# Kernel tuning notes

Measured on AMD Instinct MI355X. Metric: run time of the kernel, lower is better.

## Reference

```python
import jax, jax.numpy as jnp
import numpy as np

N_DATA, N_NODES, N_EDGES = 64, 1000, 16000


def _lrelu(x):
    return jax.nn.leaky_relu(x, 0.01)


def _mlp2(x, W1, b1, W2, b2):
    # x: [B, Cin, N] -> two 1x1-conv (per-position linear) layers with LeakyReLU
    h = _lrelu(jnp.einsum('bcn,oc->bon', x, W1) + b1[None, :, None])
    return _lrelu(jnp.einsum('bcn,oc->bon', h, W2) + b2[None, :, None])


def setup_inputs():
    key = jax.random.key(0)
    ks = jax.random.split(key, 32)
    w = lambda k, s: jax.random.normal(k, s, jnp.float32) * 0.05
    return {
        'vertices': jax.random.normal(ks[0], (N_DATA, N_NODES, 11), jnp.float32),
        'edges': jax.random.randint(ks[1], (2, N_EDGES), 0, N_NODES),
        'x_W': w(ks[2], (8, 2)), 'x_b': w(ks[3], (8,)),
        'y_W': w(ks[4], (8, 2)), 'y_b': w(ks[5], (8,)),
        'th_W': w(ks[6], (8, 2)), 'th_b': w(ks[7], (8,)),
        'cfg_W1': w(ks[8], (32, 24)), 'cfg_b1': w(ks[9], (32,)),
        'cfg_W2': w(ks[10], (32, 32)), 'cfg_b2': w(ks[11], (32,)),
        'vtx_W1': w(ks[12], (32, 64)), 'vtx_b1': w(ks[13], (32,)),
        'vtx_W2': w(ks[14], (32, 32)), 'vtx_b2': w(ks[15], (32,)),
        'edg_W1': w(ks[16], (32, 68)), 'edg_b1': w(ks[17], (32,)),
        'edg_W2': w(ks[18], (32, 32)), 'edg_b2': w(ks[19], (32,)),
        'aft_W1': w(ks[20], (32, 32)), 'aft_b1': w(ks[21], (32,)),
        'aft_W2': w(ks[22], (32, 32)), 'aft_b2': w(ks[23], (32,)),
        'vo_W1': w(ks[24], (32, 32)), 'vo_b1': w(ks[25], (32,)),
        'vo_W2': w(ks[26], (1, 32)), 'vo_b2': w(ks[27], (1,)),
        'go_W': w(ks[28], (1, N_NODES)), 'go_b': w(ks[29], (1,)),
    }


def reference(vertices, edges, x_W, x_b, y_W, y_b, th_W, th_b,
              cfg_W1, cfg_b1, cfg_W2, cfg_b2, vtx_W1, vtx_b1, vtx_W2, vtx_b2,
              edg_W1, edg_b1, edg_W2, edg_b2, aft_W1, aft_b1, aft_W2, aft_b2,
              vo_W1, vo_b1, vo_W2, vo_b2, go_W, go_b):
    n_nodes = vertices.shape[1]
    src, dst = edges[0], edges[1]

    qk, q0, qg = vertices[..., 0:3], vertices[..., 3:6], vertices[..., 6:9]
    col = jnp.transpose(vertices[..., 9:11], (0, 2, 1))  # [B, 2, N]

    def axis_feat(a, b, i, W, bb):
        # pair the i-th coordinate of two configs: [B, N, 2] -> [B, 8, N]
        p = jnp.stack([a[..., i], b[..., i]], axis=-1)
        return _lrelu(jnp.einsum('bnj,cj->bcn', p, W) + bb[None, :, None])

    def cfg_feat(other):
        f = jnp.concatenate([
            axis_feat(qk, other, 0, x_W, x_b),
            axis_feat(qk, other, 1, y_W, y_b),
            axis_feat(qk, other, 2, th_W, th_b)], axis=1)  # [B, 24, N]
        return _mlp2(f, cfg_W1, cfg_b1, cfg_W2, cfg_b2)     # [B, 32, N]

    config = jnp.concatenate([cfg_feat(q0), cfg_feat(qg)], axis=1)  # [B, 64, N]
    v = _mlp2(config, vtx_W1, vtx_b1, vtx_W2, vtx_b2)               # [B, 32, N]
    v = jnp.concatenate([v, col], axis=1)                           # [B, 34, N]

    def msgs(vf):
        # gather both endpoints, concat on channel dim, edge MLP
        pairs = jnp.concatenate([vf[:, :, src], vf[:, :, dst]], axis=1)  # [B, 68, E]
        return _mlp2(pairs, edg_W1, edg_b1, edg_W2, edg_b2)              # [B, 32, E]

    def scatter_mean(m):
        # torch: msgs.repeat((1,1,2)) scattered onto hstack(dst, src) == symmetric mean
        B, C, _ = m.shape
        sums = jnp.zeros((B, C, n_nodes), m.dtype).at[:, :, dst].add(m).at[:, :, src].add(m)
        cnt = jnp.zeros((n_nodes,), m.dtype).at[dst].add(1.0).at[src].add(1.0)
        return jnp.where(cnt > 0, sums / cnt, 0.0)

    new_vertex = scatter_mean(msgs(v))  # [B, 32, N]
    for _ in range(5):
        h = _mlp2(new_vertex, aft_W1, aft_b1, aft_W2, aft_b2)  # [B, 32, N]
        h = jnp.concatenate([h, col], axis=1)                  # [B, 34, N]
        new_vertex = new_vertex + scatter_mean(msgs(h))

    fv = _mlp2(new_vertex, vo_W1, vo_b1, vo_W2, vo_b2)[:, 0, :]  # [B, N]
    return jax.nn.sigmoid(fv @ go_W.T + go_b)                    # [B, 1]
```

## Files before the change

kernel.cpp:

```cpp
#include <hip/hip_runtime.h>
#include <hip/hip_bf16.h>
#include <cstdint>
#include <cstddef>

#define NB 64
#define NN 1000
#define NE 16000
#define ADJCAP 256

typedef __attribute__((ext_vector_type(8))) short short8;
typedef __attribute__((ext_vector_type(16))) float f32x16;

__device__ __forceinline__ float lrelu(float x) { return fmaxf(x, 0.01f * x); }

__device__ __forceinline__ float bf2f(short s) {
    unsigned int u = ((unsigned int)(unsigned short)s) << 16;
    return __builtin_bit_cast(float, u);
}
__device__ __forceinline__ short f2bf(float f) {
    __hip_bfloat16 h = __float2bfloat16(f);
    return __builtin_bit_cast(short, h);
}

union S8 { short8 v; short e[8]; };



__global__ void k_tr(const float* __restrict__ vert, float* __restrict__ vt) {
    __shared__ float s[2816];
    int n0 = blockIdx.x * 4;
    int t = threadIdx.x;
    int b = t >> 2, r = t & 3;
    const float* vp = vert + ((size_t)b * NN + n0 + r) * 11;
#pragma unroll
    for (int i = 0; i < 11; i++) s[r * 704 + i * 64 + b] = vp[i];
    __syncthreads();
    float* o = vt + (size_t)n0 * 704;
#pragma unroll
    for (int j = 0; j < 11; j++) o[j * 256 + t] = s[j * 256 + t];
}

__global__ void k_deg(const int* __restrict__ edges, int* __restrict__ deg) {
    int e = blockIdx.x * 256 + threadIdx.x;
    if (e < NE) {
        atomicAdd(&deg[edges[e]], 1);
        atomicAdd(&deg[edges[NE + e]], 1);
    }
}

__global__ void k_scan(const int* __restrict__ deg, int* __restrict__ offs,
                       int* __restrict__ cursor) {
    __shared__ int s[1024];
    int t = threadIdx.x;
    int d = (t < NN) ? deg[t] : 0;
    s[t] = d;
    __syncthreads();
    for (int k = 1; k < 1024; k <<= 1) {
        int v = (t >= k) ? s[t - k] : 0;
        __syncthreads();
        s[t] += v;
        __syncthreads();
    }
    if (t < NN) {
        offs[t + 1] = s[t];
        cursor[t] = s[t] - d;
    }
    if (t == 0) offs[0] = 0;
}

__global__ void k_fillA(const int* __restrict__ edges, int* __restrict__ cursor,
                        int* __restrict__ adj) {
    int e = blockIdx.x * 256 + threadIdx.x;
    if (e < NE) {
        int s = edges[e], d = edges[NE + e];
        int p1 = atomicAdd(&cursor[s], 1);
        adj[p1] = (e << 10) | d;
        int p2 = atomicAdd(&cursor[d], 1);
        adj[p2] = (1 << 30) | (e << 10) | s;
    }
}

__global__ void k_sort(const int* __restrict__ offs, int* __restrict__ adj,
                       int* __restrict__ cntA) {
    __shared__ int keys[4][ADJCAP];
    int w = threadIdx.x >> 6;
    int lane = threadIdx.x & 63;
    int n = blockIdx.x * 4 + w;
    int o0 = offs[n], o1 = offs[n + 1];
    int deg = o1 - o0;
    int cap = (deg < ADJCAP) ? deg : ADJCAP;
    for (int i = lane; i < cap; i += 64) keys[w][i] = adj[o0 + i];
    __syncthreads();
    if (deg <= ADJCAP) {
        for (int i = lane; i < deg; i += 64) {
            int k = keys[w][i];
            int r = 0;
            for (int j = 0; j < deg; j++) r += (keys[w][j] < k) ? 1 : 0;
            adj[o0 + r] = k;
        }
        if (lane == 0) {
            int c = 0;
            for (int j = 0; j < deg; j++) c += ((keys[w][j] >> 30) & 1) ? 0 : 1;
            cntA[n] = c;
        }
    } else if (lane == 0) {
        for (int i = o0 + 1; i < o1; i++) {
            int key = adj[i];
            int j = i - 1;
            while (j >= o0 && adj[j] > key) { adj[j + 1] = adj[j]; j--; }
            adj[j + 1] = key;
        }
        int c = 0;
        for (int i = o0; i < o1; i++) c += ((adj[i] >> 30) & 1) ? 0 : 1;
        cntA[n] = c;
    }
}

__global__ void k_wsetup2(const float* __restrict__ eW2, const float* __restrict__ eb2,
                          const float* __restrict__ aW1, const float* __restrict__ ab1,
                          const float* __restrict__ aW2, const float* __restrict__ ab2,
                          const float* __restrict__ eW1, const float* __restrict__ eb1,
                          const float* __restrict__ oW1, const float* __restrict__ ob1,
                          const float* __restrict__ xW, const float* __restrict__ xb,
                          const float* __restrict__ yW, const float* __restrict__ yb,
                          const float* __restrict__ tW, const float* __restrict__ tb,
                          const float* __restrict__ cW1, const float* __restrict__ cb1,
                          const float* __restrict__ cW2, const float* __restrict__ cb2,
                          const float* __restrict__ vW1, const float* __restrict__ vb1,
                          const float* __restrict__ vW2, const float* __restrict__ vb2,
                          char* __restrict__ wpk) {
    int l = threadIdx.x;
    int row = l & 31, kg = l >> 5;

    auto packAK = [&](const float* W, int ldw, int coff, int K, short8* dst) {
#pragma unroll
        for (int kh = 0; kh < 2; kh++) {
            S8 a;
#pragma unroll
            for (int j = 0; j < 8; j++) {
                int k = kh * 16 + kg * 8 + j;
                a.e[j] = (k < K) ? f2bf(W[row * ldw + coff + k]) : (short)0;
            }
            dst[kh * 64 + l] = a.v;
        }
    };
    packAK(eW2, 32, 0, 32, (short8*)(wpk + 0));
    packAK(aW1, 32, 0, 32, (short8*)(wpk + 2048));
    packAK(aW2, 32, 0, 32, (short8*)(wpk + 4096));
    packAK(eW1, 68, 0, 32, (short8*)(wpk + 6144));
    packAK(eW1, 68, 34, 32, (short8*)(wpk + 8192));
    packAK(oW1, 32, 0, 32, (short8*)(wpk + 10240));
    packAK(cW1, 24, 0, 24, (short8*)(wpk + 49152));
    packAK(cW2, 32, 0, 32, (short8*)(wpk + 51200));
    packAK(vW1, 64, 0, 32, (short8*)(wpk + 53248));
    packAK(vW1, 64, 32, 32, (short8*)(wpk + 55296));
    packAK(vW2, 32, 0, 32, (short8*)(wpk + 57344));

    float* B2f   = (float*)(wpk + 12288);
    float* aB1c  = (float*)(wpk + 16384);
    float* aB2c  = (float*)(wpk + 20480);
    float* eB1c  = (float*)(wpk + 24576);
    float* vo1bc = (float*)(wpk + 28672);
    float* Ea32  = (float*)(wpk + 32768);
    float* Ea33  = (float*)(wpk + 36864);
    float* Eb32  = (float*)(wpk + 40960);
    float* Eb33  = (float*)(wpk + 45056);
    float* cb1c  = (float*)(wpk + 71680);
    float* cb2c  = (float*)(wpk + 75776);
    float* vb1c  = (float*)(wpk + 79872);
    float* vb2c  = (float*)(wpk + 83968);
#pragma unroll
    for (int r = 0; r < 16; r++) {
        int rr = (r & 3) + 8 * (r >> 2) + 4 * kg;
        B2f[l * 16 + r]   = eb2[rr];
        aB1c[l * 16 + r]  = ab1[rr];
        aB2c[l * 16 + r]  = ab2[rr];
        eB1c[l * 16 + r]  = eb1[rr];
        vo1bc[l * 16 + r] = ob1[rr];
        Ea32[l * 16 + r]  = eW1[rr * 68 + 32];
        Ea33[l * 16 + r]  = eW1[rr * 68 + 33];
        Eb32[l * 16 + r]  = eW1[rr * 68 + 66];
        Eb33[l * 16 + r]  = eW1[rr * 68 + 67];
        cb1c[l * 16 + r]  = cb1[rr];
        cb2c[l * 16 + r]  = cb2[rr];
        vb1c[l * 16 + r]  = vb1[rr];
        vb2c[l * 16 + r]  = vb2[rr];
    }

    float* axW0 = (float*)(wpk + 59392);
    float* axW1 = (float*)(wpk + 63488);
    float* axb  = (float*)(wpk + 67584);
#pragma unroll
    for (int kh = 0; kh < 2; kh++) {
#pragma unroll
        for (int j = 0; j < 8; j++) {
            int k = kh * 16 + kg * 8 + j;
            int i = k >> 3, c = k & 7;
            float w0 = 0.f, w1 = 0.f, bb = 0.f;
            if (i < 3) {
                const float* W = (i == 0) ? xW : ((i == 1) ? yW : tW);
                const float* B = (i == 0) ? xb : ((i == 1) ? yb : tb);
                w0 = W[c * 2]; w1 = W[c * 2 + 1]; bb = B[c];
            }
            axW0[kh * 512 + l * 8 + j] = w0;
            axW1[kh * 512 + l * 8 + j] = w1;
            axb[kh * 512 + l * 8 + j]  = bb;
        }
    }
}

__global__ __launch_bounds__(256) void k_prep0f(
    const float* __restrict__ vt, const char* __restrict__ wpk,
    short* __restrict__ Ap, short* __restrict__ Bp) {
    __shared__ float loc4[4][1056];
    int w = threadIdx.x >> 6;
    int lane = threadIdx.x & 63;
    int lane31 = lane & 31, kg = lane >> 5, g8 = kg * 8;
    int n = blockIdx.x * 2 + (w >> 1);
    int bh = w & 1;
    int col = bh * 32 + lane31;
    float* loc = loc4[w];
    const float* vn = vt + (size_t)n * 704;

    const short8* cW1f = (const short8*)(wpk + 49152);
    const short8* cW2f = (const short8*)(wpk + 51200);
    const short8* vW1f0 = (const short8*)(wpk + 53248);
    const short8* vW1f1 = (const short8*)(wpk + 55296);
    const short8* vW2f = (const short8*)(wpk + 57344);
    const short8* eAf = (const short8*)(wpk + 6144);
    const short8* eBf = (const short8*)(wpk + 8192);
    const float* axW0 = (const float*)(wpk + 59392);
    const float* axW1 = (const float*)(wpk + 63488);
    const float* axb  = (const float*)(wpk + 67584);
    const float* cb1c = (const float*)(wpk + 71680) + lane * 16;
    const float* cb2c = (const float*)(wpk + 75776) + lane * 16;
    const float* vb1c = (const float*)(wpk + 79872) + lane * 16;
    const float* vb2c = (const float*)(wpk + 83968) + lane * 16;

    const f32x16 zero = {};

#define C2FRAG(Creg, F0, F1) do {                                              \
    _Pragma("unroll") for (int r = 0; r < 16; r++)                             \
        loc[lane31 * 33 + ((r & 3) + 8 * (r >> 2) + 4 * kg)] = Creg[r];        \
    _Pragma("unroll") for (int j = 0; j < 8; j++) {                            \
        F0.e[j] = f2bf(loc[lane31 * 33 + g8 + j]);                             \
        F1.e[j] = f2bf(loc[lane31 * 33 + 16 + g8 + j]); }                      \
} while (0)

    f32x16 V1;
#pragma unroll
    for (int r = 0; r < 16; r++) V1[r] = vb1c[r];

#pragma unroll
    for (int half = 0; half < 2; half++) {
        S8 ff0, ff1;
#pragma unroll
        for (int kh = 0; kh < 2; kh++) {
            int i = kh * 2 + kg;
            float p0 = vn[i * 64 + col];
            float p1 = vn[((half ? 6 : 3) + i) * 64 + col];
            const float* w0p = axW0 + kh * 512 + lane * 8;
            const float* w1p = axW1 + kh * 512 + lane * 8;
            const float* bp  = axb  + kh * 512 + lane * 8;
            S8 f;
#pragma unroll
            for (int j = 0; j < 8; j++) {
                float x = w0p[j] * p0 + w1p[j] * p1 + bp[j];
                f.e[j] = f2bf(fmaxf(x, 0.01f * x));
            }
            if (kh == 0) ff0 = f; else ff1 = f;
        }
        f32x16 C = __builtin_amdgcn_mfma_f32_32x32x16_bf16(cW1f[lane], ff0.v, zero, 0, 0, 0);
        C = __builtin_amdgcn_mfma_f32_32x32x16_bf16(cW1f[64 + lane], ff1.v, C, 0, 0, 0);
#pragma unroll
        for (int r = 0; r < 16; r++) { float m = C[r] + cb1c[r]; C[r] = fmaxf(m, 0.01f * m); }
        S8 hf0, hf1;
        C2FRAG(C, hf0, hf1);
        C = __builtin_amdgcn_mfma_f32_32x32x16_bf16(cW2f[lane], hf0.v, zero, 0, 0, 0);
        C = __builtin_amdgcn_mfma_f32_32x32x16_bf16(cW2f[64 + lane], hf1.v, C, 0, 0, 0);
#pragma unroll
        for (int r = 0; r < 16; r++) { float m = C[r] + cb2c[r]; C[r] = fmaxf(m, 0.01f * m); }
        S8 cf0, cf1;
        C2FRAG(C, cf0, cf1);
        const short8* vf = half ? vW1f1 : vW1f0;
        V1 = __builtin_amdgcn_mfma_f32_32x32x16_bf16(vf[lane], cf0.v, V1, 0, 0, 0);
        V1 = __builtin_amdgcn_mfma_f32_32x32x16_bf16(vf[64 + lane], cf1.v, V1, 0, 0, 0);
    }
#pragma unroll
    for (int r = 0; r < 16; r++) V1[r] = fmaxf(V1[r], 0.01f * V1[r]);
    S8 v1f0, v1f1;
    C2FRAG(V1, v1f0, v1f1);
    f32x16 V2 = __builtin_amdgcn_mfma_f32_32x32x16_bf16(vW2f[lane], v1f0.v, zero, 0, 0, 0);
    V2 = __builtin_amdgcn_mfma_f32_32x32x16_bf16(vW2f[64 + lane], v1f1.v, V2, 0, 0, 0);
#pragma unroll
    for (int r = 0; r < 16; r++) { float m = V2[r] + vb2c[r]; V2[r] = fmaxf(m, 0.01f * m); }
    S8 vf0, vf1;
    C2FRAG(V2, vf0, vf1);

    float c0 = vn[9 * 64 + col];
    float c1 = vn[10 * 64 + col];

    f32x16 SA = __builtin_amdgcn_mfma_f32_32x32x16_bf16(eAf[lane], vf0.v, zero, 0, 0, 0);
    SA = __builtin_amdgcn_mfma_f32_32x32x16_bf16(eAf[64 + lane], vf1.v, SA, 0, 0, 0);
    {
        const float* eb = (const float*)(wpk + 24576) + lane * 16;
        const float* e2 = (const float*)(wpk + 32768) + lane * 16;
        const float* e3 = (const float*)(wpk + 36864) + lane * 16;
#pragma unroll
        for (int r = 0; r < 16; r++) SA[r] += eb[r] + e2[r] * c0 + e3[r] * c1;
    }
    S8 p0, p1;
    C2FRAG(SA, p0, p1);
    ((short8*)(Ap + (size_t)n * 2048))[bh * 64 + lane] = p0.v;
    ((short8*)(Ap + (size_t)n * 2048))[(2 + bh) * 64 + lane] = p1.v;

    f32x16 SB = __builtin_amdgcn_mfma_f32_32x32x16_bf16(eBf[lane], vf0.v, zero, 0, 0, 0);
    SB = __builtin_amdgcn_mfma_f32_32x32x16_bf16(eBf[64 + lane], vf1.v, SB, 0, 0, 0);
    {
        const float* e2 = (const float*)(wpk + 40960) + lane * 16;
        const float* e3 = (const float*)(wpk + 45056) + lane * 16;
#pragma unroll
        for (int r = 0; r < 16; r++) SB[r] += e2[r] * c0 + e3[r] * c1;
    }
    C2FRAG(SB, p0, p1);
    ((short8*)(Bp + (size_t)n * 2048))[bh * 64 + lane] = p0.v;
    ((short8*)(Bp + (size_t)n * 2048))[(2 + bh) * 64 + lane] = p1.v;
#undef C2FRAG
}

#define VISIT(C0, C1, C2, C3) do {                                                        \
    S8 h10, h11;                                                                          \
    _Pragma("unroll") for (int j = 0; j < 8; j++) {                                       \
        float x0 = bfv[0][j] + bf2f(C0.e[j]); h10.e[j] = f2bf(fmaxf(x0, 0.01f * x0)); }   \
    _Pragma("unroll") for (int j = 0; j < 8; j++) {                                       \
        float x1 = bfv[2][j] + bf2f(C2.e[j]); h11.e[j] = f2bf(fmaxf(x1, 0.01f * x1)); }   \
    f32x16 d = __builtin_amdgcn_mfma_f32_32x32x16_bf16(w2f0.v, h10.v, zero, 0, 0, 0);     \
    d = __builtin_amdgcn_mfma_f32_32x32x16_bf16(w2f1.v, h11.v, d, 0, 0, 0);               \
    _Pragma("unroll") for (int r = 0; r < 16; r++) {                                      \
        float m = d[r] + b2v[r]; acc0[r] += fmaxf(m, 0.01f * m); }                        \
    _Pragma("unroll") for (int j = 0; j < 8; j++) {                                       \
        float x0 = bfv[1][j] + bf2f(C1.e[j]); h10.e[j] = f2bf(fmaxf(x0, 0.01f * x0)); }   \
    _Pragma("unroll") for (int j = 0; j < 8; j++) {                                       \
        float x1 = bfv[3][j] + bf2f(C3.e[j]); h11.e[j] = f2bf(fmaxf(x1, 0.01f * x1)); }   \
    d = __builtin_amdgcn_mfma_f32_32x32x16_bf16(w2f0.v, h10.v, zero, 0, 0, 0);            \
    d = __builtin_amdgcn_mfma_f32_32x32x16_bf16(w2f1.v, h11.v, d, 0, 0, 0);               \
    _Pragma("unroll") for (int r = 0; r < 16; r++) {                                      \
        float m = d[r] + b2v[r]; acc1[r] += fmaxf(m, 0.01f * m); }                        \
} while (0)

__global__ __launch_bounds__(256) void k_edge(
    const short* __restrict__ Apr, const short* __restrict__ Bpr,
    short* __restrict__ Apw, short* __restrict__ Bpw,
    const int* __restrict__ offs, const int* __restrict__ cntA,
    const int* __restrict__ adjg, const char* __restrict__ wpk,
    const float* __restrict__ vt, float* __restrict__ nv, float* __restrict__ fv,
    const float* __restrict__ oW2, const float* __restrict__ ob2,
    int pass0, int mode) {
    __shared__ float red[4][2112];
    __shared__ int adjl[ADJCAP];
    int n = blockIdx.x;
    int w = threadIdx.x >> 6;
    int lane = threadIdx.x & 63;
    int row = lane & 31, kg = lane >> 5;

    int off0 = offs[n], off1 = offs[n + 1];
    int deg = off1 - off0;
    int cA = cntA[n];

    for (int i = threadIdx.x; i < deg && i < ADJCAP; i += 256)
        adjl[i] = adjg[off0 + i] & 1023;
    __syncthreads();

    S8 w2f0, w2f1;
    w2f0.v = ((const short8*)wpk)[lane];
    w2f1.v = ((const short8*)wpk)[64 + lane];
    float b2v[16];
    {
        const float4* bp4 = (const float4*)((const float*)(wpk + 12288) + lane * 16);
#pragma unroll
        for (int q = 0; q < 4; q++) {
            float4 v = bp4[q];
            b2v[q * 4] = v.x; b2v[q * 4 + 1] = v.y;
            b2v[q * 4 + 2] = v.z; b2v[q * 4 + 3] = v.w;
        }
    }

    f32x16 acc0 = {};
    f32x16 acc1 = {};
    const f32x16 zero = {};

#pragma unroll
    for (int phase = 0; phase < 2; phase++) {
        const short* basePtr = phase ? Bpr : Apr;
        const short8* ogBase = (const short8*)(phase ? Apr : Bpr);
        int lstart = phase ? cA : 0;
        int lend   = phase ? deg : cA;

        float bfv[4][8];
        {
            const short8* np = (const short8*)(basePtr + (size_t)n * 2048);
#pragma unroll
            for (int f = 0; f < 4; f++) {
                S8 t; t.v = np[f * 64 + lane];
#pragma unroll
                for (int j = 0; j < 8; j++) bfv[f][j] = bf2f(t.e[j]);
            }
        }

        int li = lstart + w;
        S8 c0 = {}, c1 = {}, c2 = {}, c3 = {};
        if (li < lend) {
            int o = (li < ADJCAP) ? adjl[li] : (adjg[off0 + li] & 1023);
            const short8* op = ogBase + (size_t)o * 256;
            c0.v = op[lane]; c1.v = op[64 + lane];
            c2.v = op[128 + lane]; c3.v = op[192 + lane];
        }
        while (li < lend) {
            int ln = li + 4;
            S8 n0 = {}, n1 = {}, n2 = {}, n3 = {};
            if (ln < lend) {
                int o = (ln < ADJCAP) ? adjl[ln] : (adjg[off0 + ln] & 1023);
                const short8* op = ogBase + (size_t)o * 256;
                n0.v = op[lane]; n1.v = op[64 + lane];
                n2.v = op[128 + lane]; n3.v = op[192 + lane];
            }
            VISIT(c0, c1, c2, c3);
            c0 = n0; c1 = n1; c2 = n2; c3 = n3;
            li = ln;
        }
    }

#pragma unroll
    for (int bh = 0; bh < 2; bh++) {
        int b = bh * 32 + row;
#pragma unroll
        for (int r = 0; r < 16; r++) {
            int oc = (r & 3) + 8 * (r >> 2) + 4 * kg;
            red[w][b * 33 + oc] = bh ? acc1[r] : acc0[r];
        }
    }
    __syncthreads();

    {
        int t = threadIdx.x;
        size_t nb = (size_t)n * (NB * 32);
        float inv = (deg > 0) ? 1.f / (float)deg : 0.f;
#pragma unroll
        for (int j = 0; j < 8; j++) {
            int idx = t * 8 + j;
            int bb = idx >> 5, cc = idx & 31;
            float s;
            if (deg > 0) {
                s = (red[0][bb * 33 + cc] + red[1][bb * 33 + cc] +
                     red[2][bb * 33 + cc] + red[3][bb * 33 + cc]) * inv;
                if (!pass0) s += nv[nb + idx];
            } else {
                s = pass0 ? 0.f : nv[nb + idx];
            }
            nv[nb + idx] = s;
            red[0][bb * 33 + cc] = s;
        }
    }
    __syncthreads();

    if (w < 2) {
        int bh = w;
        int lane31 = lane & 31;
        int g8 = (lane >> 5) * 8;
        float* loc = red[2 + w];
        const float* cb;
        S8 a0, a1;

        S8 xf0, xf1;
#pragma unroll
        for (int j = 0; j < 8; j++) {
            xf0.e[j] = f2bf(red[0][(bh * 32 + lane31) * 33 + g8 + j]);
            xf1.e[j] = f2bf(red[0][(bh * 32 + lane31) * 33 + 16 + g8 + j]);
        }

        if (mode == 0) {
            a0.v = ((const short8*)(wpk + 2048))[lane];
            a1.v = ((const short8*)(wpk + 2048))[64 + lane];
            f32x16 C = {};
            C = __builtin_amdgcn_mfma_f32_32x32x16_bf16(a0.v, xf0.v, C, 0, 0, 0);
            C = __builtin_amdgcn_mfma_f32_32x32x16_bf16(a1.v, xf1.v, C, 0, 0, 0);
            cb = (const float*)(wpk + 16384) + lane * 16;
#pragma unroll
            for (int r = 0; r < 16; r++) { float m = C[r] + cb[r]; C[r] = fmaxf(m, 0.01f * m); }
#pragma unroll
            for (int r = 0; r < 16; r++) {
                int oc = (r & 3) + 8 * (r >> 2) + 4 * kg;
                loc[lane31 * 33 + oc] = C[r];
            }
            S8 hf0, hf1;
#pragma unroll
            for (int j = 0; j < 8; j++) {
                hf0.e[j] = f2bf(loc[lane31 * 33 + g8 + j]);
                hf1.e[j] = f2bf(loc[lane31 * 33 + 16 + g8 + j]);
            }
            a0.v = ((const short8*)(wpk + 4096))[lane];
            a1.v = ((const short8*)(wpk + 4096))[64 + lane];
            f32x16 V = {};
            V = __builtin_amdgcn_mfma_f32_32x32x16_bf16(a0.v, hf0.v, V, 0, 0, 0);
            V = __builtin_amdgcn_mfma_f32_32x32x16_bf16(a1.v, hf1.v, V, 0, 0, 0);
            cb = (const float*)(wpk + 20480) + lane * 16;
#pragma unroll
            for (int r = 0; r < 16; r++) { float m = V[r] + cb[r]; V[r] = fmaxf(m, 0.01f * m); }
#pragma unroll
            for (int r = 0; r < 16; r++) {
                int oc = (r & 3) + 8 * (r >> 2) + 4 * kg;
                loc[lane31 * 33 + oc] = V[r];
            }
            S8 vf0, vf1;
#pragma unroll
            for (int j = 0; j < 8; j++) {
                vf0.e[j] = f2bf(loc[lane31 * 33 + g8 + j]);
                vf1.e[j] = f2bf(loc[lane31 * 33 + 16 + g8 + j]);
            }
            float c0 = vt[(size_t)n * 704 + 9 * 64 + bh * 32 + lane31];
            float c1 = vt[(size_t)n * 704 + 10 * 64 + bh * 32 + lane31];

            a0.v = ((const short8*)(wpk + 6144))[lane];
            a1.v = ((const short8*)(wpk + 6144))[64 + lane];
            f32x16 SA = {};
            SA = __builtin_amdgcn_mfma_f32_32x32x16_bf16(a0.v, vf0.v, SA, 0, 0, 0);
            SA = __builtin_amdgcn_mfma_f32_32x32x16_bf16(a1.v, vf1.v, SA, 0, 0, 0);
            {
                const float* eb = (const float*)(wpk + 24576) + lane * 16;
                const float* e2 = (const float*)(wpk + 32768) + lane * 16;
                const float* e3 = (const float*)(wpk + 36864) + lane * 16;
#pragma unroll
                for (int r = 0; r < 16; r++) SA[r] += eb[r] + e2[r] * c0 + e3[r] * c1;
            }
#pragma unroll
            for (int r = 0; r < 16; r++) {
                int oc = (r & 3) + 8 * (r >> 2) + 4 * kg;
                loc[lane31 * 33 + oc] = SA[r];
            }
            {
                S8 p0, p1;
#pragma unroll
                for (int j = 0; j < 8; j++) {
                    p0.e[j] = f2bf(loc[lane31 * 33 + g8 + j]);
                    p1.e[j] = f2bf(loc[lane31 * 33 + 16 + g8 + j]);
                }
                ((short8*)(Apw + (size_t)n * 2048))[bh * 64 + lane] = p0.v;
                ((short8*)(Apw + (size_t)n * 2048))[(2 + bh) * 64 + lane] = p1.v;
            }
            a0.v = ((const short8*)(wpk + 8192))[lane];
            a1.v = ((const short8*)(wpk + 8192))[64 + lane];
            f32x16 SB = {};
            SB = __builtin_amdgcn_mfma_f32_32x32x16_bf16(a0.v, vf0.v, SB, 0, 0, 0);
            SB = __builtin_amdgcn_mfma_f32_32x32x16_bf16(a1.v, vf1.v, SB, 0, 0, 0);
            {
                const float* e2 = (const float*)(wpk + 40960) + lane * 16;
                const float* e3 = (const float*)(wpk + 45056) + lane * 16;
#pragma unroll
                for (int r = 0; r < 16; r++) SB[r] += e2[r] * c0 + e3[r] * c1;
            }
#pragma unroll
            for (int r = 0; r < 16; r++) {
                int oc = (r & 3) + 8 * (r >> 2) + 4 * kg;
                loc[lane31 * 33 + oc] = SB[r];
            }
            {
                S8 p0, p1;
#pragma unroll
                for (int j = 0; j < 8; j++) {
                    p0.e[j] = f2bf(loc[lane31 * 33 + g8 + j]);
                    p1.e[j] = f2bf(loc[lane31 * 33 + 16 + g8 + j]);
                }
                ((short8*)(Bpw + (size_t)n * 2048))[bh * 64 + lane] = p0.v;
                ((short8*)(Bpw + (size_t)n * 2048))[(2 + bh) * 64 + lane] = p1.v;
            }
        } else {
            a0.v = ((const short8*)(wpk + 10240))[lane];
            a1.v = ((const short8*)(wpk + 10240))[64 + lane];
            f32x16 C = {};
            C = __builtin_amdgcn_mfma_f32_32x32x16_bf16(a0.v, xf0.v, C, 0, 0, 0);
            C = __builtin_amdgcn_mfma_f32_32x32x16_bf16(a1.v, xf1.v, C, 0, 0, 0);
            cb = (const float*)(wpk + 28672) + lane * 16;
#pragma unroll
            for (int r = 0; r < 16; r++) { float m = C[r] + cb[r]; C[r] = fmaxf(m, 0.01f * m); }
#pragma unroll
            for (int r = 0; r < 16; r++) {
                int oc = (r & 3) + 8 * (r >> 2) + 4 * kg;
                loc[lane31 * 33 + oc] = C[r];
            }
            float s = 0.f;
#pragma unroll
            for (int o = 0; o < 16; o++) {
                int oc = (lane >> 5) * 16 + o;
                s += oW2[oc] * loc[lane31 * 33 + oc];
            }
            s += __shfl_xor(s, 32);
            if (lane < 32) {
                float v = s + ob2[0];
                fv[n * 64 + bh * 32 + lane31] = fmaxf(v, 0.01f * v);
            }
        }
    }
}

__global__ void k_final2(const float* __restrict__ fv, const float* __restrict__ gW,
                         const float* __restrict__ gb, float* __restrict__ out) {
    int b = blockIdx.x;
    int t = threadIdx.x;
    float part = 0.f;
    for (int n = t; n < NN; n += 256) part += fv[n * 64 + b] * gW[n];
    __shared__ float rs[256];
    rs[t] = part;
    __syncthreads();
    for (int d = 128; d > 0; d >>= 1) {
        if (t < d) rs[t] += rs[t + d];
        __syncthreads();
    }
    if (t == 0) out[b] = 1.f / (1.f + expf(-(rs[0] + gb[0])));
}

extern "C" void kernel_launch(void* const* d_in, const int* in_sizes, int n_in,
                              void* d_out, int out_size, void* d_ws, size_t ws_size,
                              hipStream_t stream) {
    (void)in_sizes; (void)n_in; (void)out_size; (void)ws_size;
    const float* vert = (const float*)d_in[0];
    const int* edges  = (const int*)d_in[1];
    const float* xW   = (const float*)d_in[2];
    const float* xb   = (const float*)d_in[3];
    const float* yW   = (const float*)d_in[4];
    const float* yb   = (const float*)d_in[5];
    const float* tW   = (const float*)d_in[6];
    const float* tb   = (const float*)d_in[7];
    const float* cW1  = (const float*)d_in[8];
    const float* cb1  = (const float*)d_in[9];
    const float* cW2  = (const float*)d_in[10];
    const float* cb2  = (const float*)d_in[11];
    const float* vW1  = (const float*)d_in[12];
    const float* vb1  = (const float*)d_in[13];
    const float* vW2  = (const float*)d_in[14];
    const float* vb2  = (const float*)d_in[15];
    const float* eW1  = (const float*)d_in[16];
    const float* eb1  = (const float*)d_in[17];
    const float* eW2  = (const float*)d_in[18];
    const float* eb2  = (const float*)d_in[19];
    const float* aW1  = (const float*)d_in[20];
    const float* ab1  = (const float*)d_in[21];
    const float* aW2  = (const float*)d_in[22];
    const float* ab2  = (const float*)d_in[23];
    const float* oW1  = (const float*)d_in[24];
    const float* ob1  = (const float*)d_in[25];
    const float* oW2  = (const float*)d_in[26];
    const float* ob2  = (const float*)d_in[27];
    const float* gW   = (const float*)d_in[28];
    const float* gb   = (const float*)d_in[29];
    float* out = (float*)d_out;

    char* w = (char*)d_ws;
    short* ApA = (short*)(w + 0);
    short* BpA = (short*)(w + (4u << 20));
    short* ApB = (short*)(w + (8u << 20));
    short* BpB = (short*)(w + (12u << 20));
    float* nv  = (float*)(w + (16u << 20));
    float* vt  = (float*)(w + (25u << 20));
    float* fv  = (float*)(w + (28u << 20));
    char*  wpk = w + (28u << 20) + (512u << 10);
    int* deg    = (int*)(w + (29u << 20));
    int* offs   = deg + 1024;
    int* cursor = offs + 1024;
    int* cntA   = cursor + 1024;
    int* adj    = cntA + 1024;

    hipMemsetAsync(deg, 0, NN * sizeof(int), stream);
    k_tr<<<NN / 4, 256, 0, stream>>>(vert, vt);
    k_deg<<<(NE + 255) / 256, 256, 0, stream>>>(edges, deg);
    k_scan<<<1, 1024, 0, stream>>>(deg, offs, cursor);
    k_fillA<<<(NE + 255) / 256, 256, 0, stream>>>(edges, cursor, adj);
    k_sort<<<NN / 4, 256, 0, stream>>>(offs, adj, cntA);
    k_wsetup2<<<1, 64, 0, stream>>>(eW2, eb2, aW1, ab1, aW2, ab2, eW1, eb1, oW1, ob1,
                                    xW, xb, yW, yb, tW, tb, cW1, cb1, cW2, cb2,
                                    vW1, vb1, vW2, vb2, wpk);

    k_prep0f<<<NN / 2, 256, 0, stream>>>(vt, wpk, ApA, BpA);

    short* bufs[2][2] = {{ApA, BpA}, {ApB, BpB}};
    for (int p = 0; p < 6; p++) {
        int rb = p & 1, wb = rb ^ 1;
        int mode = (p == 5) ? 1 : 0;
        int pass0 = (p == 0) ? 1 : 0;
        k_edge<<<NN, 256, 0, stream>>>(bufs[rb][0], bufs[rb][1],
                                       bufs[wb][0], bufs[wb][1],
                                       offs, cntA, adj, wpk, vt, nv, fv,
                                       oW2, ob2, pass0, mode);
    }

    k_final2<<<NB, 256, 0, stream>>>(fv, gW, gb, out);
}
```

Measured before the change: 303.3 us.

## Switch bf16 MFMA path to fp16 with packed half lrelu and deeper prefetch

Stores all packed weights and activations as fp16 instead of bf16 and uses the fp16 MFMA instruction. In the edge loop, the per-element bf16-to-float conversions and float LeakyReLU are replaced by packed half8 add/mul/max ops. The neighbor prefetch goes from one edge ahead to two, using alternating A/B register sets. The deg memset is folded into k_tr, removing one launch. This trades fp16 range limits and extra register pressure for fewer conversion ALU ops and more latency hiding.

```diff
diff --git a/kernel.cpp b/kernel.cpp
--- a/kernel.cpp
+++ b/kernel.cpp
@@ -1,5 +1,5 @@
 #include <hip/hip_runtime.h>
-#include <hip/hip_bf16.h>
+#include <hip/hip_fp16.h>
 #include <cstdint>
 #include <cstddef>
 
@@ -9,27 +9,28 @@
 #define ADJCAP 256
 
 typedef __attribute__((ext_vector_type(8))) short short8;
+typedef __attribute__((ext_vector_type(8))) _Float16 half8;
 typedef __attribute__((ext_vector_type(16))) float f32x16;
 
 __device__ __forceinline__ float lrelu(float x) { return fmaxf(x, 0.01f * x); }
 
-__device__ __forceinline__ float bf2f(short s) {
-    unsigned int u = ((unsigned int)(unsigned short)s) << 16;
-    return __builtin_bit_cast(float, u);
-}
-__device__ __forceinline__ short f2bf(float f) {
-    __hip_bfloat16 h = __float2bfloat16(f);
-    return __builtin_bit_cast(short, h);
-}
-
-union S8 { short8 v; short e[8]; };
-
-
-
-__global__ void k_tr(const float* __restrict__ vert, float* __restrict__ vt) {
+union S8 { short8 v; half8 h; _Float16 e[8]; unsigned int u[4]; };
+
+__device__ __forceinline__ half8 h8lreluadd(half8 a, half8 b) {
+    half8 x = a + b;
+    half8 y = x * (_Float16)0.01f;
+    return __builtin_elementwise_max(x, y);
+}
+
+
+
+__global__ void k_tr(const float* __restrict__ vert, float* __restrict__ vt,
+                     int* __restrict__ deg) {
     __shared__ float s[2816];
     int n0 = blockIdx.x * 4;
     int t = threadIdx.x;
+    if (blockIdx.x == 0)
+        for (int i = t; i < 1024; i += 256) deg[i] = 0;
     int b = t >> 2, r = t & 3;
     const float* vp = vert + ((size_t)b * NN + n0 + r) * 11;
 #pragma unroll
@@ -139,7 +140,7 @@
 #pragma unroll
             for (int j = 0; j < 8; j++) {
                 int k = kh * 16 + kg * 8 + j;
-                a.e[j] = (k < K) ? f2bf(W[row * ldw + coff + k]) : (short)0;
+                a.e[j] = (k < K) ? (_Float16)W[row * ldw + coff + k] : (_Float16)0.f;
             }
             dst[kh * 64 + l] = a.v;
         }
@@ -243,8 +244,8 @@
     _Pragma("unroll") for (int r = 0; r < 16; r++)                             \
         loc[lane31 * 33 + ((r & 3) + 8 * (r >> 2) + 4 * kg)] = Creg[r];        \
     _Pragma("unroll") for (int j = 0; j < 8; j++) {                            \
-        F0.e[j] = f2bf(loc[lane31 * 33 + g8 + j]);                             \
-        F1.e[j] = f2bf(loc[lane31 * 33 + 16 + g8 + j]); }                      \
+        F0.e[j] = (_Float16)loc[lane31 * 33 + g8 + j];                         \
+        F1.e[j] = (_Float16)loc[lane31 * 33 + 16 + g8 + j]; }                  \
 } while (0)
 
     f32x16 V1;
@@ -266,32 +267,36 @@
 #pragma unroll
             for (int j = 0; j < 8; j++) {
                 float x = w0p[j] * p0 + w1p[j] * p1 + bp[j];
-                f.e[j] = f2bf(fmaxf(x, 0.01f * x));
+                f.e[j] = (_Float16)fmaxf(x, 0.01f * x);
             }
             if (kh == 0) ff0 = f; else ff1 = f;
         }
-        f32x16 C = __builtin_amdgcn_mfma_f32_32x32x16_bf16(cW1f[lane], ff0.v, zero, 0, 0, 0);
-        C = __builtin_amdgcn_mfma_f32_32x32x16_bf16(cW1f[64 + lane], ff1.v, C, 0, 0, 0);
+        S8 cw0, cw1; cw0.v = cW1f[lane]; cw1.v = cW1f[64 + lane];
+        f32x16 C = __builtin_amdgcn_mfma_f32_32x32x16_f16(cw0.h, ff0.h, zero, 0, 0, 0);
+        C = __builtin_amdgcn_mfma_f32_32x32x16_f16(cw1.h, ff1.h, C, 0, 0, 0);
 #pragma unroll
         for (int r = 0; r < 16; r++) { float m = C[r] + cb1c[r]; C[r] = fmaxf(m, 0.01f * m); }
         S8 hf0, hf1;
         C2FRAG(C, hf0, hf1);
-        C = __builtin_amdgcn_mfma_f32_32x32x16_bf16(cW2f[lane], hf0.v, zero, 0, 0, 0);
-        C = __builtin_amdgcn_mfma_f32_32x32x16_bf16(cW2f[64 + lane], hf1.v, C, 0, 0, 0);
+        cw0.v = cW2f[lane]; cw1.v = cW2f[64 + lane];
+        C = __builtin_amdgcn_mfma_f32_32x32x16_f16(cw0.h, hf0.h, zero, 0, 0, 0);
+        C = __builtin_amdgcn_mfma_f32_32x32x16_f16(cw1.h, hf1.h, C, 0, 0, 0);
 #pragma unroll
         for (int r = 0; r < 16; r++) { float m = C[r] + cb2c[r]; C[r] = fmaxf(m, 0.01f * m); }
         S8 cf0, cf1;
         C2FRAG(C, cf0, cf1);
         const short8* vf = half ? vW1f1 : vW1f0;
-        V1 = __builtin_amdgcn_mfma_f32_32x32x16_bf16(vf[lane], cf0.v, V1, 0, 0, 0);
-        V1 = __builtin_amdgcn_mfma_f32_32x32x16_bf16(vf[64 + lane], cf1.v, V1, 0, 0, 0);
+        S8 vw0, vw1; vw0.v = vf[lane]; vw1.v = vf[64 + lane];
+        V1 = __builtin_amdgcn_mfma_f32_32x32x16_f16(vw0.h, cf0.h, V1, 0, 0, 0);
+        V1 = __builtin_amdgcn_mfma_f32_32x32x16_f16(vw1.h, cf1.h, V1, 0, 0, 0);
     }
 #pragma unroll
     for (int r = 0; r < 16; r++) V1[r] = fmaxf(V1[r], 0.01f * V1[r]);
     S8 v1f0, v1f1;
     C2FRAG(V1, v1f0, v1f1);
-    f32x16 V2 = __builtin_amdgcn_mfma_f32_32x32x16_bf16(vW2f[lane], v1f0.v, zero, 0, 0, 0);
-    V2 = __builtin_amdgcn_mfma_f32_32x32x16_bf16(vW2f[64 + lane], v1f1.v, V2, 0, 0, 0);
+    S8 vw0, vw1; vw0.v = vW2f[lane]; vw1.v = vW2f[64 + lane];
+    f32x16 V2 = __builtin_amdgcn_mfma_f32_32x32x16_f16(vw0.h, v1f0.h, zero, 0, 0, 0);
+    V2 = __builtin_amdgcn_mfma_f32_32x32x16_f16(vw1.h, v1f1.h, V2, 0, 0, 0);
 #pragma unroll
     for (int r = 0; r < 16; r++) { float m = V2[r] + vb2c[r]; V2[r] = fmaxf(m, 0.01f * m); }
     S8 vf0, vf1;
@@ -300,8 +305,9 @@
     float c0 = vn[9 * 64 + col];
     float c1 = vn[10 * 64 + col];
 
-    f32x16 SA = __builtin_amdgcn_mfma_f32_32x32x16_bf16(eAf[lane], vf0.v, zero, 0, 0, 0);
-    SA = __builtin_amdgcn_mfma_f32_32x32x16_bf16(eAf[64 + lane], vf1.v, SA, 0, 0, 0);
+    S8 ea0, ea1; ea0.v = eAf[lane]; ea1.v = eAf[64 + lane];
+    f32x16 SA = __builtin_amdgcn_mfma_f32_32x32x16_f16(ea0.h, vf0.h, zero, 0, 0, 0);
+    SA = __builtin_amdgcn_mfma_f32_32x32x16_f16(ea1.h, vf1.h, SA, 0, 0, 0);
     {
         const float* eb = (const float*)(wpk + 24576) + lane * 16;
         const float* e2 = (const float*)(wpk + 32768) + lane * 16;
@@ -314,8 +320,9 @@
     ((short8*)(Ap + (size_t)n * 2048))[bh * 64 + lane] = p0.v;
     ((short8*)(Ap + (size_t)n * 2048))[(2 + bh) * 64 + lane] = p1.v;
 
-    f32x16 SB = __builtin_amdgcn_mfma_f32_32x32x16_bf16(eBf[lane], vf0.v, zero, 0, 0, 0);
-    SB = __builtin_amdgcn_mfma_f32_32x32x16_bf16(eBf[64 + lane], vf1.v, SB, 0, 0, 0);
+    S8 eb0, eb1f; eb0.v = eBf[lane]; eb1f.v = eBf[64 + lane];
+    f32x16 SB = __builtin_amdgcn_mfma_f32_32x32x16_f16(eb0.h, vf0.h, zero, 0, 0, 0);
+    SB = __builtin_amdgcn_mfma_f32_32x32x16_f16(eb1f.h, vf1.h, SB, 0, 0, 0);
     {
         const float* e2 = (const float*)(wpk + 40960) + lane * 16;
         const float* e3 = (const float*)(wpk + 45056) + lane * 16;
@@ -328,24 +335,27 @@
 #undef C2FRAG
 }
 
-#define VISIT(C0, C1, C2, C3) do {                                                        \
+#define VISITH(C0, C1, C2, C3) do {                                                       \
     S8 h10, h11;                                                                          \
-    _Pragma("unroll") for (int j = 0; j < 8; j++) {                                       \
-        float x0 = bfv[0][j] + bf2f(C0.e[j]); h10.e[j] = f2bf(fmaxf(x0, 0.01f * x0)); }   \
-    _Pragma("unroll") for (int j = 0; j < 8; j++) {                                       \
-        float x1 = bfv[2][j] + bf2f(C2.e[j]); h11.e[j] = f2bf(fmaxf(x1, 0.01f * x1)); }   \
-    f32x16 d = __builtin_amdgcn_mfma_f32_32x32x16_bf16(w2f0.v, h10.v, zero, 0, 0, 0);     \
-    d = __builtin_amdgcn_mfma_f32_32x32x16_bf16(w2f1.v, h11.v, d, 0, 0, 0);               \
+    h10.h = h8lreluadd(ba0.h, C0.h);                                                      \
+    h11.h = h8lreluadd(ba2.h, C2.h);                                                      \
+    f32x16 d = __builtin_amdgcn_mfma_f32_32x32x16_f16(w2f0.h, h10.h, zero, 0, 0, 0);      \
+    d = __builtin_amdgcn_mfma_f32_32x32x16_f16(w2f1.h, h11.h, d, 0, 0, 0);                \
     _Pragma("unroll") for (int r = 0; r < 16; r++) {                                      \
         float m = d[r] + b2v[r]; acc0[r] += fmaxf(m, 0.01f * m); }                        \
-    _Pragma("unroll") for (int j = 0; j < 8; j++) {                                       \
-        float x0 = bfv[1][j] + bf2f(C1.e[j]); h10.e[j] = f2bf(fmaxf(x0, 0.01f * x0)); }   \
-    _Pragma("unroll") for (int j = 0; j < 8; j++) {                                       \
-        float x1 = bfv[3][j] + bf2f(C3.e[j]); h11.e[j] = f2bf(fmaxf(x1, 0.01f * x1)); }   \
-    d = __builtin_amdgcn_mfma_f32_32x32x16_bf16(w2f0.v, h10.v, zero, 0, 0, 0);            \
-    d = __builtin_amdgcn_mfma_f32_32x32x16_bf16(w2f1.v, h11.v, d, 0, 0, 0);               \
+    h10.h = h8lreluadd(ba1.h, C1.h);                                                      \
+    h11.h = h8lreluadd(ba3.h, C3.h);                                                      \
+    d = __builtin_amdgcn_mfma_f32_32x32x16_f16(w2f0.h, h10.h, zero, 0, 0, 0);             \
+    d = __builtin_amdgcn_mfma_f32_32x32x16_f16(w2f1.h, h11.h, d, 0, 0, 0);                \
     _Pragma("unroll") for (int r = 0; r < 16; r++) {                                      \
         float m = d[r] + b2v[r]; acc1[r] += fmaxf(m, 0.01f * m); }                        \
+} while (0)
+
+#define LOADO(P0, P1, P2, P3, idx) do {                                                   \
+    int o_ = ((idx) < ADJCAP) ? adjl[idx] : (adjg[off0 + (idx)] & 1023);                  \
+    const short8* op_ = ogBase + (size_t)o_ * 256;                                        \
+    P0.v = op_[lane]; P1.v = op_[64 + lane];                                              \
+    P2.v = op_[128 + lane]; P3.v = op_[192 + lane];                                       \
 } while (0)
 
 __global__ __launch_bounds__(256) void k_edge(
@@ -396,37 +406,36 @@
         int lstart = phase ? cA : 0;
         int lend   = phase ? deg : cA;
 
-        float bfv[4][8];
+        S8 ba0, ba1, ba2, ba3;
         {
             const short8* np = (const short8*)(basePtr + (size_t)n * 2048);
-#pragma unroll
-            for (int f = 0; f < 4; f++) {
-                S8 t; t.v = np[f * 64 + lane];
-#pragma unroll
-                for (int j = 0; j < 8; j++) bfv[f][j] = bf2f(t.e[j]);
-            }
+            ba0.v = np[lane]; ba1.v = np[64 + lane];
+            ba2.v = np[128 + lane]; ba3.v = np[192 + lane];
         }
 
         int li = lstart + w;
-        S8 c0 = {}, c1 = {}, c2 = {}, c3 = {};
-        if (li < lend) {
-            int o = (li < ADJCAP) ? adjl[li] : (adjg[off0 + li] & 1023);
-            const short8* op = ogBase + (size_t)o * 256;
-            c0.v = op[lane]; c1.v = op[64 + lane];
-            c2.v = op[128 + lane]; c3.v = op[192 + lane];
-        }
+        S8 A0 = {}, A1 = {}, A2 = {}, A3 = {};
+        S8 B0 = {}, B1 = {}, B2 = {}, B3 = {};
+        if (li < lend) LOADO(A0, A1, A2, A3, li);
+        if (li + 4 < lend) LOADO(B0, B1, B2, B3, li + 4);
         while (li < lend) {
-            int ln = li + 4;
-            S8 n0 = {}, n1 = {}, n2 = {}, n3 = {};
-            if (ln < lend) {
-                int o = (ln < ADJCAP) ? adjl[ln] : (adjg[off0 + ln] & 1023);
-                const short8* op = ogBase + (size_t)o * 256;
-                n0.v = op[lane]; n1.v = op[64 + lane];
-                n2.v = op[128 + lane]; n3.v = op[192 + lane];
-            }
-            VISIT(c0, c1, c2, c3);
-            c0 = n0; c1 = n1; c2 = n2; c3 = n3;
-            li = ln;
+            {
+                int lp = li + 8;
+                S8 n0 = {}, n1 = {}, n2 = {}, n3 = {};
+                if (lp < lend) LOADO(n0, n1, n2, n3, lp);
+                VISITH(A0, A1, A2, A3);
+                A0 = n0; A1 = n1; A2 = n2; A3 = n3;
+            }
+            li += 4;
+            if (li >= lend) break;
+            {
+                int lp = li + 8;
+                S8 n0 = {}, n1 = {}, n2 = {}, n3 = {};
+                if (lp < lend) LOADO(n0, n1, n2, n3, lp);
+                VISITH(B0, B1, B2, B3);
+                B0 = n0; B1 = n1; B2 = n2; B3 = n3;
+            }
+            li += 4;
         }
     }
 
@@ -474,16 +483,16 @@
         S8 xf0, xf1;
 #pragma unroll
         for (int j = 0; j < 8; j++) {
-            xf0.e[j] = f2bf(red[0][(bh * 32 + lane31) * 33 + g8 + j]);
-            xf1.e[j] = f2bf(red[0][(bh * 32 + lane31) * 33 + 16 + g8 + j]);
+            xf0.e[j] = (_Float16)red[0][(bh * 32 + lane31) * 33 + g8 + j];
+            xf1.e[j] = (_Float16)red[0][(bh * 32 + lane31) * 33 + 16 + g8 + j];
         }
 
         if (mode == 0) {
             a0.v = ((const short8*)(wpk + 2048))[lane];
             a1.v = ((const short8*)(wpk + 2048))[64 + lane];
             f32x16 C = {};
-            C = __builtin_amdgcn_mfma_f32_32x32x16_bf16(a0.v, xf0.v, C, 0, 0, 0);
-            C = __builtin_amdgcn_mfma_f32_32x32x16_bf16(a1.v, xf1.v, C, 0, 0, 0);
+            C = __builtin_amdgcn_mfma_f32_32x32x16_f16(a0.h, xf0.h, C, 0, 0, 0);
+            C = __builtin_amdgcn_mfma_f32_32x32x16_f16(a1.h, xf1.h, C, 0, 0, 0);
             cb = (const float*)(wpk + 16384) + lane * 16;
 #pragma unroll
             for (int r = 0; r < 16; r++) { float m = C[r] + cb[r]; C[r] = fmaxf(m, 0.01f * m); }
@@ -495,14 +504,14 @@
             S8 hf0, hf1;
 #pragma unroll
             for (int j = 0; j < 8; j++) {
-                hf0.e[j] = f2bf(loc[lane31 * 33 + g8 + j]);
-                hf1.e[j] = f2bf(loc[lane31 * 33 + 16 + g8 + j]);
+                hf0.e[j] = (_Float16)loc[lane31 * 33 + g8 + j];
+                hf1.e[j] = (_Float16)loc[lane31 * 33 + 16 + g8 + j];
             }
             a0.v = ((const short8*)(wpk + 4096))[lane];
             a1.v = ((const short8*)(wpk + 4096))[64 + lane];
             f32x16 V = {};
-            V = __builtin_amdgcn_mfma_f32_32x32x16_bf16(a0.v, hf0.v, V, 0, 0, 0);
-            V = __builtin_amdgcn_mfma_f32_32x32x16_bf16(a1.v, hf1.v, V, 0, 0, 0);
+            V = __builtin_amdgcn_mfma_f32_32x32x16_f16(a0.h, hf0.h, V, 0, 0, 0);
+            V = __builtin_amdgcn_mfma_f32_32x32x16_f16(a1.h, hf1.h, V, 0, 0, 0);
             cb = (const float*)(wpk + 20480) + lane * 16;
 #pragma unroll
             for (int r = 0; r < 16; r++) { float m = V[r] + cb[r]; V[r] = fmaxf(m, 0.01f * m); }
@@ -514,8 +523,8 @@
             S8 vf0, vf1;
 #pragma unroll
             for (int j = 0; j < 8; j++) {
-                vf0.e[j] = f2bf(loc[lane31 * 33 + g8 + j]);
-                vf1.e[j] = f2bf(loc[lane31 * 33 + 16 + g8 + j]);
+                vf0.e[j] = (_Float16)loc[lane31 * 33 + g8 + j];
+                vf1.e[j] = (_Float16)loc[lane31 * 33 + 16 + g8 + j];
             }
             float c0 = vt[(size_t)n * 704 + 9 * 64 + bh * 32 + lane31];
             float c1 = vt[(size_t)n * 704 + 10 * 64 + bh * 32 + lane31];
@@ -523,8 +532,8 @@
             a0.v = ((const short8*)(wpk + 6144))[lane];
             a1.v = ((const short8*)(wpk + 6144))[64 + lane];
             f32x16 SA = {};
-            SA = __builtin_amdgcn_mfma_f32_32x32x16_bf16(a0.v, vf0.v, SA, 0, 0, 0);
-            SA = __builtin_amdgcn_mfma_f32_32x32x16_bf16(a1.v, vf1.v, SA, 0, 0, 0);
+            SA = __builtin_amdgcn_mfma_f32_32x32x16_f16(a0.h, vf0.h, SA, 0, 0, 0);
+            SA = __builtin_amdgcn_mfma_f32_32x32x16_f16(a1.h, vf1.h, SA, 0, 0, 0);
             {
                 const float* eb = (const float*)(wpk + 24576) + lane * 16;
                 const float* e2 = (const float*)(wpk + 32768) + lane * 16;
@@ -541,8 +550,8 @@
                 S8 p0, p1;
 #pragma unroll
                 for (int j = 0; j < 8; j++) {
-                    p0.e[j] = f2bf(loc[lane31 * 33 + g8 + j]);
-                    p1.e[j] = f2bf(loc[lane31 * 33 + 16 + g8 + j]);
+                    p0.e[j] = (_Float16)loc[lane31 * 33 + g8 + j];
+                    p1.e[j] = (_Float16)loc[lane31 * 33 + 16 + g8 + j];
                 }
                 ((short8*)(Apw + (size_t)n * 2048))[bh * 64 + lane] = p0.v;
                 ((short8*)(Apw + (size_t)n * 2048))[(2 + bh) * 64 + lane] = p1.v;
@@ -550,8 +559,8 @@
             a0.v = ((const short8*)(wpk + 8192))[lane];
             a1.v = ((const short8*)(wpk + 8192))[64 + lane];
             f32x16 SB = {};
-            SB = __builtin_amdgcn_mfma_f32_32x32x16_bf16(a0.v, vf0.v, SB, 0, 0, 0);
-            SB = __builtin_amdgcn_mfma_f32_32x32x16_bf16(a1.v, vf1.v, SB, 0, 0, 0);
+            SB = __builtin_amdgcn_mfma_f32_32x32x16_f16(a0.h, vf0.h, SB, 0, 0, 0);
+            SB = __builtin_amdgcn_mfma_f32_32x32x16_f16(a1.h, vf1.h, SB, 0, 0, 0);
             {
                 const float* e2 = (const float*)(wpk + 40960) + lane * 16;
                 const float* e3 = (const float*)(wpk + 45056) + lane * 16;
@@ -567,8 +576,8 @@
                 S8 p0, p1;
 #pragma unroll
                 for (int j = 0; j < 8; j++) {
-                    p0.e[j] = f2bf(loc[lane31 * 33 + g8 + j]);
-                    p1.e[j] = f2bf(loc[lane31 * 33 + 16 + g8 + j]);
+                    p0.e[j] = (_Float16)loc[lane31 * 33 + g8 + j];
+                    p1.e[j] = (_Float16)loc[lane31 * 33 + 16 + g8 + j];
                 }
                 ((short8*)(Bpw + (size_t)n * 2048))[bh * 64 + lane] = p0.v;
                 ((short8*)(Bpw + (size_t)n * 2048))[(2 + bh) * 64 + lane] = p1.v;
@@ -577,8 +586,8 @@
             a0.v = ((const short8*)(wpk + 10240))[lane];
             a1.v = ((const short8*)(wpk + 10240))[64 + lane];
             f32x16 C = {};
-            C = __builtin_amdgcn_mfma_f32_32x32x16_bf16(a0.v, xf0.v, C, 0, 0, 0);
-            C = __builtin_amdgcn_mfma_f32_32x32x16_bf16(a1.v, xf1.v, C, 0, 0, 0);
+            C = __builtin_amdgcn_mfma_f32_32x32x16_f16(a0.h, xf0.h, C, 0, 0, 0);
+            C = __builtin_amdgcn_mfma_f32_32x32x16_f16(a1.h, xf1.h, C, 0, 0, 0);
             cb = (const float*)(wpk + 28672) + lane * 16;
 #pragma unroll
             for (int r = 0; r < 16; r++) { float m = C[r] + cb[r]; C[r] = fmaxf(m, 0.01f * m); }
@@ -669,8 +678,7 @@
     int* cntA   = cursor + 1024;
     int* adj    = cntA + 1024;
 
-    hipMemsetAsync(deg, 0, NN * sizeof(int), stream);
-    k_tr<<<NN / 4, 256, 0, stream>>>(vert, vt);
+    k_tr<<<NN / 4, 256, 0, stream>>>(vert, vt, deg);
     k_deg<<<(NE + 255) / 256, 256, 0, stream>>>(edges, deg);
     k_scan<<<1, 1024, 0, stream>>>(deg, offs, cursor);
     k_fillA<<<(NE + 255) / 256, 256, 0, stream>>>(edges, cursor, adj);
```

Result: faster. 291.8 us (-3.8%).
